# Optimization experiments

Measured on AMD Instinct MI355X. Metric: run time of the kernel, lower is better.

## Reference

```python
import jax, jax.numpy as jnp
import numpy as np

N = 50000   # nodes
E = 800000  # edges
IN = 128
H = 256
OUT = 10
G = 128     # graphs in batch


def _uniform(key, shape, fan_in):
    bound = 1.0 / np.sqrt(fan_in)
    return jax.random.uniform(key, shape, jnp.float32, -bound, bound)


def setup_inputs() -> dict:
    key = jax.random.key(0)
    ks = jax.random.split(key, 12)
    x = jax.random.normal(ks[0], (N, IN), jnp.float32)
    edge_index = jax.random.randint(ks[1], (2, E), 0, N, dtype=jnp.int64)
    edge_weight = jax.random.uniform(ks[2], (E,), jnp.float32)
    batch = jnp.sort(jax.random.randint(ks[3], (N,), 0, G, dtype=jnp.int64))
    # GCNConv weights (bias=False)
    W0 = _uniform(ks[4], (IN, H), IN)
    W1 = _uniform(ks[5], (H, H), H)
    W2 = _uniform(ks[6], (H, H), H)
    # MLP head: [H, H, OUT]
    Wm1 = _uniform(ks[7], (H, H), H)
    bm1 = _uniform(ks[8], (H,), H)
    Wm2 = _uniform(ks[9], (H, OUT), H)
    bm2 = _uniform(ks[10], (OUT,), H)
    return dict(x=x, edge_index=edge_index, edge_weight=edge_weight, batch=batch,
                W0=W0, W1=W1, W2=W2, Wm1=Wm1, bm1=bm1, Wm2=Wm2, bm2=bm2)


def _gcn_conv(h, W, row, col, dinv_sqrt):
    """GCNConv with self-loops and symmetric deg^-1/2 normalization, bias=False.
    Self-loop contribution handled analytically (norm = dinv_sqrt[i]^2)."""
    hw = h @ W                                        # [N, H]
    norm = dinv_sqrt[row] * dinv_sqrt[col]            # [E]
    msg = hw[row] * norm[:, None]                     # [E, H] gather-scale
    agg = jax.ops.segment_sum(msg, col, num_segments=N)  # scatter-add at targets
    return agg + (dinv_sqrt * dinv_sqrt)[:, None] * hw    # add self-loop term


def reference(x, edge_index, edge_weight, batch, W0, W1, W2, Wm1, bm1, Wm2, bm2):
    row, col = edge_index[0], edge_index[1]
    # degree including self-loop (edge_weight is ignored, as in the source)
    deg = jax.ops.segment_sum(jnp.ones((E,), x.dtype), col, num_segments=N) + 1.0
    dinv_sqrt = jax.lax.rsqrt(deg)
    h = x
    for W in (W0, W1, W2):
        h = jax.nn.relu(_gcn_conv(h, W, row, col, dinv_sqrt))
    # global mean pool over graphs
    counts = jax.ops.segment_sum(jnp.ones((N,), h.dtype), batch, num_segments=G)
    pooled = jax.ops.segment_sum(h, batch, num_segments=G) / jnp.maximum(counts, 1.0)[:, None]
    # MLP head (dropout inactive at inference)
    hmid = jax.nn.relu(pooled @ Wm1 + bm1)
    last = hmid @ Wm2 + bm2
    return jax.nn.log_softmax(last, axis=-1), jax.nn.sigmoid(last), last
```

## Files before the change

### kernel.cpp

```cpp
#include <hip/hip_runtime.h>
#include <math.h>

#define N_NODES 50000
#define N_PAD   50048
#define N_EDGES 800000
#define CSR_CAP 1200000
#define IN_F 128
#define H_F 256
#define OUT_F 10
#define N_G 128
#define NCHUNKS 196

#define HB 256
#define EPB (N_EDGES / HB)
#define HWORDS (N_NODES / 4)

typedef __attribute__((ext_vector_type(4))) float f32x4;
typedef __attribute__((ext_vector_type(2))) float f32x2;
typedef unsigned char u8;

__device__ inline f32x2 fp8x2_f32_lo(unsigned int v) {
    return __builtin_amdgcn_cvt_pk_f32_fp8(v, false);
}
__device__ inline f32x2 fp8x2_f32_hi(unsigned int v) {
    return __builtin_amdgcn_cvt_pk_f32_fp8(v, true);
}
__device__ inline unsigned int f32_fp8x2_lo(float a, float b, unsigned int old) {
    return __builtin_amdgcn_cvt_pk_fp8_f32(a, b, old, false);
}
__device__ inline unsigned int f32_fp8x2_hi(float a, float b, unsigned int old) {
    return __builtin_amdgcn_cvt_pk_fp8_f32(a, b, old, true);
}
__device__ inline u8 f32_fp8(float a) {
    return (u8)(f32_fp8x2_lo(a, a, 0u) & 0xff);
}
__device__ inline ushort f2bf(float x) {
    union { float f; unsigned int u; } v; v.f = x;
    unsigned int r = v.u + 0x7fff + ((v.u >> 16) & 1);
    return (ushort)(r >> 16);
}
__device__ inline float bf2f(ushort u) {
    union { unsigned int u; float f; } v; v.u = ((unsigned int)u) << 16; return v.f;
}

__device__ inline void gl2lds16(const void* g, void* l) {
    __builtin_amdgcn_global_load_lds(
        (const __attribute__((address_space(1))) unsigned int*)g,
        (__attribute__((address_space(3))) unsigned int*)l,
        16, 0, 0);
}

__global__ __launch_bounds__(256) void histo_kernel(const int* __restrict__ col,
                                                    u8* __restrict__ H) {
    extern __shared__ unsigned int hcnt[];
    int b = blockIdx.x;
    int tid = threadIdx.x;
    for (int j = tid; j < HWORDS; j += 256) hcnt[j] = 0u;
    __syncthreads();
    int e0 = b * EPB, e1 = e0 + EPB;
    for (int e = e0 + tid; e < e1; e += 512) {
        int c0 = col[e];
        int c1 = (e + 256 < e1) ? col[e + 256] : -1;
        atomicAdd(&hcnt[c0 >> 2], 1u << ((c0 & 3) << 3));
        if (c1 >= 0) atomicAdd(&hcnt[c1 >> 2], 1u << ((c1 & 3) << 3));
    }
    __syncthreads();
    unsigned int* Hrow = (unsigned int*)(H + (size_t)b * N_NODES);
    for (int j = tid; j < HWORDS; j += 256) Hrow[j] = hcnt[j];
}

#define CC_CHUNK 196
#define CC_X    (CC_CHUNK + 6250)
#define CC_T0   (CC_X + 128)
#define CC_T1   (CC_T0 + 256)
#define CC_T2   (CC_T1 + 256)
#define CC_GS   (CC_T2 + NCHUNKS)

__global__ __launch_bounds__(256) void convert_chunk_kernel(
    u8* __restrict__ H, int* __restrict__ counts, int* __restrict__ csum,
    const float* __restrict__ x, u8* __restrict__ xb,
    const float* __restrict__ W0, u8* __restrict__ W0t,
    const float* __restrict__ W1, u8* __restrict__ W1t,
    const float* __restrict__ W2, u8* __restrict__ W2t,
    const int* __restrict__ batch, int* __restrict__ gstart) {
    int b = blockIdx.x;
    int tid = threadIdx.x;
    if (b < CC_CHUNK) {
        int i = b * 256 + tid;
        int total = 0;
        if (i < N_NODES) {
            u8* ci = H + i;
            int s = 0;
            for (int b0 = 0; b0 < HB; b0 += 16) {
                int h[16];
                #pragma unroll
                for (int u = 0; u < 16; ++u)
                    h[u] = ci[(size_t)(b0 + u) * N_NODES];
                #pragma unroll
                for (int u = 0; u < 16; ++u) {
                    ci[(size_t)(b0 + u) * N_NODES] = (u8)s;
                    s += h[u];
                }
            }
            total = s;
            counts[i] = total;
        }
        int v = (i < N_NODES) ? ((total + 7) & ~7) : 0;
        #pragma unroll
        for (int off = 32; off; off >>= 1) v += __shfl_down(v, off);
        __shared__ int ws[4];
        if ((tid & 63) == 0) ws[tid >> 6] = v;
        __syncthreads();
        if (tid == 0) csum[b] = ws[0] + ws[1] + ws[2] + ws[3];
    } else if (b < CC_X) {
        int i = (b - CC_CHUNK) * 256 + tid;
        float4 v = *(const float4*)(x + (size_t)i * 4);
        unsigned int p = f32_fp8x2_lo(v.x, v.y, 0u);
        p = f32_fp8x2_hi(v.z, v.w, p);
        *(unsigned int*)(xb + (size_t)i * 4) = p;
    } else if (b < CC_T0) {
        int idx = (b - CC_X) * 256 + tid;
        int k = idx >> 8, nn = idx & 255;
        W0t[nn * IN_F + k] = f32_fp8(W0[idx]);
    } else if (b < CC_T1) {
        int idx = (b - CC_T0) * 256 + tid;
        int k = idx >> 8, nn = idx & 255;
        W1t[nn * H_F + k] = f32_fp8(W1[idx]);
    } else if (b < CC_T2) {
        int idx = (b - CC_T1) * 256 + tid;
        int k = idx >> 8, nn = idx & 255;
        W2t[nn * H_F + k] = f32_fp8(W2[idx]);
    } else {
        int i = (b - CC_T2) * 256 + tid;
        if (i >= N_NODES) return;
        int bb = batch[i];
        if (i == 0) {
            for (int g = 0; g <= bb; ++g) gstart[g] = 0;
        } else {
            int p = batch[i - 1];
            if (p != bb) { for (int g = p + 1; g <= bb; ++g) gstart[g] = i; }
        }
        if (i == N_NODES - 1) {
            for (int g = bb + 1; g <= N_G; ++g) gstart[g] = N_NODES;
        }
    }
}

__global__ __launch_bounds__(256) void scan_dinv_kernel(const int* __restrict__ counts,
                                                        const int* __restrict__ csum,
                                                        int* __restrict__ offsets,
                                                        float* __restrict__ dinv,
                                                        unsigned int* __restrict__ csr_ew,
                                                        int n) {
    int tid = threadIdx.x;
    int lane = tid & 63, wid = tid >> 6;
    int cv = (tid < NCHUNKS) ? csum[tid] : 0;
    int xc = cv;
    #pragma unroll
    for (int off = 1; off < 64; off <<= 1) {
        int t = __shfl_up(xc, off);
        if (lane >= off) xc += t;
    }
    __shared__ int cw[4], cpre[4];
    __shared__ int cexcl[257];
    if (lane == 63) cw[wid] = xc;
    __syncthreads();
    if (tid == 0) { int s = 0; for (int k = 0; k < 4; ++k) { cpre[k] = s; s += cw[k]; } }
    __syncthreads();
    cexcl[tid] = cpre[wid] + xc - cv;
    if (tid == 255) cexcl[256] = cpre[3] + cw[3];
    __syncthreads();
    int base = cexcl[blockIdx.x];
    int i = blockIdx.x * 256 + tid;
    int v = (i < n) ? counts[i] : 0;
    int pv = (v + 7) & ~7;
    int x = pv;
    #pragma unroll
    for (int off = 1; off < 64; off <<= 1) {
        int t = __shfl_up(x, off);
        if (lane >= off) x += t;
    }
    __shared__ int wsum[4], wpre[4];
    if (lane == 63) wsum[wid] = x;
    __syncthreads();
    if (tid == 0) { int s = 0; for (int k = 0; k < 4; ++k) { wpre[k] = s; s += wsum[k]; } }
    __syncthreads();
    if (i < n) {
        int o = base + wpre[wid] + x - pv;
        offsets[i] = o;
        dinv[i] = rsqrtf((float)(v + 1));
        for (int z = v; z < pv; ++z) csr_ew[o + z] = 0u;
    }
    if (blockIdx.x == 0 && tid == 0) offsets[n] = cexcl[NCHUNKS];
}

__global__ __launch_bounds__(256) void fill_csr_kernel(const int* __restrict__ row,
                                                       const int* __restrict__ col,
                                                       const int* __restrict__ offsets,
                                                       const u8* __restrict__ H,
                                                       const float* __restrict__ dinv,
                                                       unsigned int* __restrict__ csr_ew) {
    extern __shared__ unsigned int hl[];
    int b = blockIdx.x;
    int tid = threadIdx.x;
    const unsigned int* Hrow = (const unsigned int*)(H + (size_t)b * N_NODES);
    for (int j = tid; j < HWORDS; j += 256) hl[j] = Hrow[j];
    __syncthreads();
    int e0 = b * EPB, e1 = e0 + EPB;
    for (int e = e0 + tid; e < e1; e += 512) {
        int eb = e + 256;
        int c0 = col[e];
        int r0 = row[e];
        int c1 = -1, r1 = 0;
        if (eb < e1) { c1 = col[eb]; r1 = row[eb]; }
        float w0 = dinv[c0] * dinv[r0];
        float w1 = (c1 >= 0) ? dinv[c1] * dinv[r1] : 0.f;
        int sh0 = (c0 & 3) << 3;
        unsigned int old0 = atomicAdd(&hl[c0 >> 2], 1u << sh0);
        int k0 = (int)((old0 >> sh0) & 0xffu);
        csr_ew[offsets[c0] + k0] = (unsigned int)r0 | ((unsigned int)f2bf(w0) << 16);
        if (c1 >= 0) {
            int sh1 = (c1 & 3) << 3;
            unsigned int old1 = atomicAdd(&hl[c1 >> 2], 1u << sh1);
            int k1 = (int)((old1 >> sh1) & 0xffu);
            csr_ew[offsets[c1] + k1] = (unsigned int)r1 | ((unsigned int)f2bf(w1) << 16);
        }
    }
}

template <int K, bool RELU>
__global__ __launch_bounds__(256) void gemm_fp8(const u8* __restrict__ A,
                                                const u8* __restrict__ Bt,
                                                u8* __restrict__ C) {
    __shared__ u8 As[4 * 4096];
    __shared__ u8 Bs[4 * 4096];
    int tid = threadIdx.x;
    int lane = tid & 63;
    int w = tid >> 6;
    int wm = w & 1, wn = w >> 1;
    int l16 = lane & 15, quad = lane >> 4;
    int row0 = blockIdx.x * 128;
    int col0 = blockIdx.y * 128;
    f32x4 acc[4][4] = {};

    int sr = tid >> 1;
    int sh = (tid & 1) * 16;
    const u8* ga = A + (size_t)(row0 + sr) * K + sh;
    const u8* gb = Bt + (size_t)(col0 + sr) * K + sh;

    #pragma unroll
    for (int k0 = 0; k0 < K; k0 += 128) {
        if (k0) __syncthreads();
        #pragma unroll
        for (int q = 0; q < 4; ++q) {
            gl2lds16(ga + k0 + q * 32, As + q * 4096 + w * 1024);
            gl2lds16(gb + k0 + q * 32, Bs + q * 4096 + w * 1024);
        }
        __syncthreads();
        #pragma unroll
        for (int h = 0; h < 4; ++h) {
            long af[4], bfr[4];
            #pragma unroll
            for (int i = 0; i < 4; ++i)
                af[i] = *(const long*)&As[h * 4096 + (wm * 64 + i * 16 + l16) * 32 + quad * 8];
            #pragma unroll
            for (int j = 0; j < 4; ++j)
                bfr[j] = *(const long*)&Bs[h * 4096 + (wn * 64 + j * 16 + l16) * 32 + quad * 8];
            #pragma unroll
            for (int i = 0; i < 4; ++i)
                #pragma unroll
                for (int j = 0; j < 4; ++j)
                    acc[i][j] = __builtin_amdgcn_mfma_f32_16x16x32_fp8_fp8(af[i], bfr[j], acc[i][j], 0, 0, 0);
        }
    }
    #pragma unroll
    for (int i = 0; i < 4; ++i) {
        int rowb = row0 + wm * 64 + i * 16 + quad * 4;
        #pragma unroll
        for (int r = 0; r < 4; ++r) {
            int grow = rowb + r;
            #pragma unroll
            for (int j = 0; j < 4; ++j) {
                int gcol = col0 + wn * 64 + j * 16 + l16;
                float v = acc[i][j][r];
                if (RELU) v = fmaxf(v, 0.f);
                C[(size_t)grow * H_F + gcol] = f32_fp8(v);
            }
        }
    }
}

__global__ __launch_bounds__(256) void aggregate128(const u8* __restrict__ hw,
                                                    const float* __restrict__ dinv,
                                                    const int* __restrict__ offsets,
                                                    const unsigned int* __restrict__ csr_ew,
                                                    u8* __restrict__ hout) {
    int w = threadIdx.x >> 6;
    int lane = threadIdx.x & 63;
    int i = blockIdx.x * 4 + w;
    if (i >= N_NODES) return;
    float di = dinv[i];
    const u8* base = hw + (size_t)lane * 2;
    unsigned int su = *(const unsigned short*)(base + (size_t)i * IN_F);
    f32x2 sv = fp8x2_f32_lo(su);
    float s = di * di;
    float a0 = s * sv.x, a1 = s * sv.y;
    int t = __builtin_amdgcn_readfirstlane(offsets[i]);
    int end = __builtin_amdgcn_readfirstlane(offsets[i + 1]);
    if (t < end) {
        uint4 eA = *(const uint4*)(csr_ew + t);
        uint4 eB = *(const uint4*)(csr_ew + t + 4);
        for (; t < end; t += 8) {
            uint4 nA, nB;
            if (t + 8 < end) {
                nA = *(const uint4*)(csr_ew + t + 8);
                nB = *(const uint4*)(csr_ew + t + 12);
            }
            unsigned int e[8] = {eA.x, eA.y, eA.z, eA.w, eB.x, eB.y, eB.z, eB.w};
            unsigned int v[8];
            #pragma unroll
            for (int u = 0; u < 8; ++u)
                v[u] = *(const unsigned short*)(base + (size_t)(e[u] & 0xffff) * IN_F);
            #pragma unroll
            for (int u = 0; u < 8; ++u) {
                float wq = bf2f((ushort)(e[u] >> 16));
                f32x2 f = fp8x2_f32_lo(v[u]);
                a0 += wq * f.x; a1 += wq * f.y;
            }
            eA = nA; eB = nB;
        }
    }
    unsigned int o = f32_fp8x2_lo(a0, a1, 0u);
    *(unsigned short*)(hout + (size_t)i * IN_F + lane * 2) = (unsigned short)(o & 0xffff);
}

__global__ __launch_bounds__(256) void aggregate256(const u8* __restrict__ hw,
                                                    const float* __restrict__ dinv,
                                                    const int* __restrict__ offsets,
                                                    const unsigned int* __restrict__ csr_ew,
                                                    u8* __restrict__ hout) {
    int w = threadIdx.x >> 6;
    int lane = threadIdx.x & 63;
    int i = blockIdx.x * 4 + w;
    if (i >= N_NODES) return;
    float di = dinv[i];
    const u8* base = hw + (size_t)lane * 4;
    unsigned int su = *(const unsigned int*)(base + (size_t)i * H_F);
    f32x2 slo = fp8x2_f32_lo(su), shi = fp8x2_f32_hi(su);
    float s = di * di;
    float a0 = s * slo.x, a1 = s * slo.y, a2 = s * shi.x, a3 = s * shi.y;
    int t = __builtin_amdgcn_readfirstlane(offsets[i]);
    int end = __builtin_amdgcn_readfirstlane(offsets[i + 1]);
    if (t < end) {
        uint4 eA = *(const uint4*)(csr_ew + t);
        uint4 eB = *(const uint4*)(csr_ew + t + 4);
        for (; t < end; t += 8) {
            uint4 nA, nB;
            if (t + 8 < end) {
                nA = *(const uint4*)(csr_ew + t + 8);
                nB = *(const uint4*)(csr_ew + t + 12);
            }
            unsigned int e[8] = {eA.x, eA.y, eA.z, eA.w, eB.x, eB.y, eB.z, eB.w};
            unsigned int v[8];
            #pragma unroll
            for (int u = 0; u < 8; ++u)
                v[u] = *(const unsigned int*)(base + (size_t)(e[u] & 0xffff) * H_F);
            #pragma unroll
            for (int u = 0; u < 8; ++u) {
                float wq = bf2f((ushort)(e[u] >> 16));
                f32x2 lo = fp8x2_f32_lo(v[u]), hi = fp8x2_f32_hi(v[u]);
                a0 += wq * lo.x; a1 += wq * lo.y;
                a2 += wq * hi.x; a3 += wq * hi.y;
            }
            eA = nA; eB = nB;
        }
    }
    unsigned int o = f32_fp8x2_lo(fmaxf(a0, 0.f), fmaxf(a1, 0.f), 0u);
    o = f32_fp8x2_hi(fmaxf(a2, 0.f), fmaxf(a3, 0.f), o);
    *(unsigned int*)(hout + (size_t)i * H_F + lane * 4) = o;
}

__global__ __launch_bounds__(1024) void pool_mlp_kernel(const u8* __restrict__ h,
                                                        const int* __restrict__ gstart,
                                                        const float* __restrict__ Wm1,
                                                        const float* __restrict__ bm1,
                                                        const float* __restrict__ Wm2,
                                                        const float* __restrict__ bm2,
                                                        float* __restrict__ out) {
    __shared__ float sm[16][H_F];
    __shared__ float p[H_F];
    __shared__ float hmid[H_F];
    __shared__ float lastv[OUT_F];
    __shared__ float stats[2];
    int g = blockIdx.x;
    int s = gstart[g], e = gstart[g + 1];
    int w = threadIdx.x >> 6;
    int lane = threadIdx.x & 63;
    float a0 = 0.f, a1 = 0.f, a2 = 0.f, a3 = 0.f;
    for (int i = s + w; i < e; i += 16) {
        unsigned int v = *(const unsigned int*)(h + (size_t)i * H_F + lane * 4);
        f32x2 lo = fp8x2_f32_lo(v), hi = fp8x2_f32_hi(v);
        a0 += lo.x; a1 += lo.y; a2 += hi.x; a3 += hi.y;
    }
    *(f32x4*)&sm[w][lane * 4] = (f32x4){a0, a1, a2, a3};
    __syncthreads();
    int j = threadIdx.x;
    int cnt = e - s;
    if (j < H_F) {
        float t = 0.f;
        #pragma unroll
        for (int k = 0; k < 16; ++k) t += sm[k][j];
        p[j] = t / (float)max(cnt, 1);
    }
    __syncthreads();
    if (j < H_F) {
        float acc = bm1[j];
        for (int k = 0; k < H_F; ++k) acc += p[k] * Wm1[k * H_F + j];
        hmid[j] = fmaxf(acc, 0.f);
    }
    __syncthreads();
    if (j < OUT_F) {
        float a = bm2[j];
        for (int k = 0; k < H_F; ++k) a += hmid[k] * Wm2[k * OUT_F + j];
        lastv[j] = a;
    }
    __syncthreads();
    if (j == 0) {
        float m = -1e30f;
        for (int o = 0; o < OUT_F; ++o) m = fmaxf(m, lastv[o]);
        float sxp = 0.f;
        for (int o = 0; o < OUT_F; ++o) sxp += expf(lastv[o] - m);
        stats[0] = m; stats[1] = logf(sxp);
    }
    __syncthreads();
    if (j < OUT_F) {
        float v = lastv[j];
        out[g * OUT_F + j] = v - stats[0] - stats[1];
        out[(size_t)N_G * OUT_F + g * OUT_F + j] = 1.f / (1.f + expf(-v));
        out[(size_t)2 * N_G * OUT_F + g * OUT_F + j] = v;
    }
}

extern "C" void kernel_launch(void* const* d_in, const int* in_sizes, int n_in,
                              void* d_out, int out_size, void* d_ws, size_t ws_size,
                              hipStream_t stream) {
    const float* x   = (const float*)d_in[0];
    const int* edge_index = (const int*)d_in[1];
    const int* batch = (const int*)d_in[3];
    const float* W0  = (const float*)d_in[4];
    const float* W1  = (const float*)d_in[5];
    const float* W2  = (const float*)d_in[6];
    const float* Wm1 = (const float*)d_in[7];
    const float* bm1 = (const float*)d_in[8];
    const float* Wm2 = (const float*)d_in[9];
    const float* bm2 = (const float*)d_in[10];
    float* out = (float*)d_out;

    char* ws = (char*)d_ws;
    size_t off = 0;
    auto alloc = [&](size_t bytes) -> void* {
        void* p = ws + off; off += (bytes + 255) & ~(size_t)255; return p;
    };
    u8* xb       = (u8*)alloc((size_t)N_PAD * IN_F);
    u8* bufA     = (u8*)alloc((size_t)N_PAD * H_F);
    u8* bufB     = (u8*)alloc((size_t)N_PAD * H_F);
    u8* t0       = (u8*)alloc((size_t)N_PAD * IN_F);
    u8* W0t      = (u8*)alloc((size_t)H_F * IN_F);
    u8* W1t      = (u8*)alloc((size_t)H_F * H_F);
    u8* W2t      = (u8*)alloc((size_t)H_F * H_F);
    float* dinv    = (float*)alloc((size_t)N_NODES * 4);
    int*   counts  = (int*)alloc((size_t)N_NODES * 4);
    int*   offsets = (int*)alloc((size_t)(N_NODES + 1) * 4);
    u8*    H       = (u8*)alloc((size_t)HB * N_NODES);
    unsigned int* csr_ew = (unsigned int*)alloc((size_t)CSR_CAP * 4);
    int*   csum    = (int*)alloc((size_t)256 * 4);
    int*   gstart  = (int*)alloc((size_t)(N_G + 1) * 4);

    const int* row = edge_index;
    const int* col = edge_index + N_EDGES;

    histo_kernel<<<HB, 256, HWORDS * 4, stream>>>(col, H);
    convert_chunk_kernel<<<CC_GS, 256, 0, stream>>>(H, counts, csum, x, xb,
                                                    W0, W0t, W1, W1t, W2, W2t,
                                                    batch, gstart);
    scan_dinv_kernel<<<NCHUNKS, 256, 0, stream>>>(counts, csum, offsets, dinv,
                                                  csr_ew, N_NODES);
    fill_csr_kernel<<<HB, 256, HWORDS * 4, stream>>>(row, col, offsets, H,
                                                     dinv, csr_ew);

    dim3 gg(N_PAD / 128, H_F / 128);
    int agg_blocks = (N_NODES + 3) / 4;
    aggregate128<<<agg_blocks, 256, 0, stream>>>(xb, dinv, offsets, csr_ew, t0);
    gemm_fp8<IN_F, true><<<gg, 256, 0, stream>>>(t0, W0t, bufA);
    gemm_fp8<H_F, false><<<gg, 256, 0, stream>>>(bufA, W1t, bufB);
    aggregate256<<<agg_blocks, 256, 0, stream>>>(bufB, dinv, offsets, csr_ew, bufA);
    gemm_fp8<H_F, false><<<gg, 256, 0, stream>>>(bufA, W2t, bufB);
    aggregate256<<<agg_blocks, 256, 0, stream>>>(bufB, dinv, offsets, csr_ew, bufA);

    pool_mlp_kernel<<<N_G, 1024, 0, stream>>>(bufA, gstart, Wm1, bm1, Wm2, bm2, out);
}
```

Measured before the change: 267.6 us.

## Fuse CSR build kernels into one cooperative kernel with grid syncs

```diff
diff --git a/kernel.cpp b/kernel.cpp
--- a/kernel.cpp
+++ b/kernel.cpp
@@ -1,5 +1,8 @@
 #include <hip/hip_runtime.h>
+#include <hip/hip_cooperative_groups.h>
 #include <math.h>
+
+namespace cg = cooperative_groups;
 
 #define N_NODES 50000
 #define N_PAD   50048
@@ -14,6 +17,13 @@
 #define HB 256
 #define EPB (N_EDGES / HB)
 #define HWORDS (N_NODES / 4)
+#define COOP_GRID 512
+
+#define U_X   6250
+#define U_W0  (U_X + 128)
+#define U_W1  (U_W0 + 256)
+#define U_W2  (U_W1 + 256)
+#define U_GS  (U_W2 + NCHUNKS)
 
 typedef __attribute__((ext_vector_type(4))) float f32x4;
 typedef __attribute__((ext_vector_type(2))) float f32x2;
@@ -50,42 +60,75 @@
         16, 0, 0);
 }
 
-__global__ __launch_bounds__(256) void histo_kernel(const int* __restrict__ col,
-                                                    u8* __restrict__ H) {
-    extern __shared__ unsigned int hcnt[];
-    int b = blockIdx.x;
-    int tid = threadIdx.x;
-    for (int j = tid; j < HWORDS; j += 256) hcnt[j] = 0u;
-    __syncthreads();
-    int e0 = b * EPB, e1 = e0 + EPB;
-    for (int e = e0 + tid; e < e1; e += 512) {
-        int c0 = col[e];
-        int c1 = (e + 256 < e1) ? col[e + 256] : -1;
-        atomicAdd(&hcnt[c0 >> 2], 1u << ((c0 & 3) << 3));
-        if (c1 >= 0) atomicAdd(&hcnt[c1 >> 2], 1u << ((c1 & 3) << 3));
-    }
-    __syncthreads();
-    unsigned int* Hrow = (unsigned int*)(H + (size_t)b * N_NODES);
-    for (int j = tid; j < HWORDS; j += 256) Hrow[j] = hcnt[j];
-}
-
-#define CC_CHUNK 196
-#define CC_X    (CC_CHUNK + 6250)
-#define CC_T0   (CC_X + 128)
-#define CC_T1   (CC_T0 + 256)
-#define CC_T2   (CC_T1 + 256)
-#define CC_GS   (CC_T2 + NCHUNKS)
-
-__global__ __launch_bounds__(256) void convert_chunk_kernel(
+__global__ __launch_bounds__(256) void csr_build_kernel(
+    const int* __restrict__ col, const int* __restrict__ rowp,
     u8* __restrict__ H, int* __restrict__ counts, int* __restrict__ csum,
+    int* __restrict__ offsets, float* __restrict__ dinv,
+    unsigned int* __restrict__ csr_ew,
     const float* __restrict__ x, u8* __restrict__ xb,
     const float* __restrict__ W0, u8* __restrict__ W0t,
     const float* __restrict__ W1, u8* __restrict__ W1t,
     const float* __restrict__ W2, u8* __restrict__ W2t,
     const int* __restrict__ batch, int* __restrict__ gstart) {
+    extern __shared__ unsigned int lds[];
+    cg::grid_group grid = cg::this_grid();
     int b = blockIdx.x;
     int tid = threadIdx.x;
-    if (b < CC_CHUNK) {
+
+    if (b < HB) {
+        for (int j = tid; j < HWORDS; j += 256) lds[j] = 0u;
+        __syncthreads();
+        int e0 = b * EPB, e1 = e0 + EPB;
+        for (int e = e0 + tid; e < e1; e += 512) {
+            int c0 = col[e];
+            int c1 = (e + 256 < e1) ? col[e + 256] : -1;
+            atomicAdd(&lds[c0 >> 2], 1u << ((c0 & 3) << 3));
+            if (c1 >= 0) atomicAdd(&lds[c1 >> 2], 1u << ((c1 & 3) << 3));
+        }
+        __syncthreads();
+        unsigned int* Hrow = (unsigned int*)(H + (size_t)b * N_NODES);
+        for (int j = tid; j < HWORDS; j += 256) Hrow[j] = lds[j];
+    } else {
+        for (int unit = b - HB; unit < U_GS; unit += (COOP_GRID - HB)) {
+            if (unit < U_X) {
+                int i = unit * 256 + tid;
+                float4 v = *(const float4*)(x + (size_t)i * 4);
+                unsigned int p = f32_fp8x2_lo(v.x, v.y, 0u);
+                p = f32_fp8x2_hi(v.z, v.w, p);
+                *(unsigned int*)(xb + (size_t)i * 4) = p;
+            } else if (unit < U_W0) {
+                int idx = (unit - U_X) * 256 + tid;
+                int k = idx >> 8, nn = idx & 255;
+                W0t[nn * IN_F + k] = f32_fp8(W0[idx]);
+            } else if (unit < U_W1) {
+                int idx = (unit - U_W0) * 256 + tid;
+                int k = idx >> 8, nn = idx & 255;
+                W1t[nn * H_F + k] = f32_fp8(W1[idx]);
+            } else if (unit < U_W2) {
+                int idx = (unit - U_W1) * 256 + tid;
+                int k = idx >> 8, nn = idx & 255;
+                W2t[nn * H_F + k] = f32_fp8(W2[idx]);
+            } else {
+                int i = (unit - U_W2) * 256 + tid;
+                if (i < N_NODES) {
+                    int bb = batch[i];
+                    if (i == 0) {
+                        for (int g = 0; g <= bb; ++g) gstart[g] = 0;
+                    } else {
+                        int p = batch[i - 1];
+                        if (p != bb) { for (int g = p + 1; g <= bb; ++g) gstart[g] = i; }
+                    }
+                    if (i == N_NODES - 1) {
+                        for (int g = bb + 1; g <= N_G; ++g) gstart[g] = N_NODES;
+                    }
+                }
+            }
+        }
+    }
+    __threadfence();
+    grid.sync();
+
+    if (b < NCHUNKS) {
         int i = b * 256 + tid;
         int total = 0;
         if (i < N_NODES) {
@@ -112,118 +155,77 @@
         if ((tid & 63) == 0) ws[tid >> 6] = v;
         __syncthreads();
         if (tid == 0) csum[b] = ws[0] + ws[1] + ws[2] + ws[3];
-    } else if (b < CC_X) {
-        int i = (b - CC_CHUNK) * 256 + tid;
-        float4 v = *(const float4*)(x + (size_t)i * 4);
-        unsigned int p = f32_fp8x2_lo(v.x, v.y, 0u);
-        p = f32_fp8x2_hi(v.z, v.w, p);
-        *(unsigned int*)(xb + (size_t)i * 4) = p;
-    } else if (b < CC_T0) {
-        int idx = (b - CC_X) * 256 + tid;
-        int k = idx >> 8, nn = idx & 255;
-        W0t[nn * IN_F + k] = f32_fp8(W0[idx]);
-    } else if (b < CC_T1) {
-        int idx = (b - CC_T0) * 256 + tid;
-        int k = idx >> 8, nn = idx & 255;
-        W1t[nn * H_F + k] = f32_fp8(W1[idx]);
-    } else if (b < CC_T2) {
-        int idx = (b - CC_T1) * 256 + tid;
-        int k = idx >> 8, nn = idx & 255;
-        W2t[nn * H_F + k] = f32_fp8(W2[idx]);
-    } else {
-        int i = (b - CC_T2) * 256 + tid;
-        if (i >= N_NODES) return;
-        int bb = batch[i];
-        if (i == 0) {
-            for (int g = 0; g <= bb; ++g) gstart[g] = 0;
-        } else {
-            int p = batch[i - 1];
-            if (p != bb) { for (int g = p + 1; g <= bb; ++g) gstart[g] = i; }
-        }
-        if (i == N_NODES - 1) {
-            for (int g = bb + 1; g <= N_G; ++g) gstart[g] = N_NODES;
-        }
-    }
-}
-
-__global__ __launch_bounds__(256) void scan_dinv_kernel(const int* __restrict__ counts,
-                                                        const int* __restrict__ csum,
-                                                        int* __restrict__ offsets,
-                                                        float* __restrict__ dinv,
-                                                        unsigned int* __restrict__ csr_ew,
-                                                        int n) {
-    int tid = threadIdx.x;
-    int lane = tid & 63, wid = tid >> 6;
-    int cv = (tid < NCHUNKS) ? csum[tid] : 0;
-    int xc = cv;
-    #pragma unroll
-    for (int off = 1; off < 64; off <<= 1) {
-        int t = __shfl_up(xc, off);
-        if (lane >= off) xc += t;
-    }
-    __shared__ int cw[4], cpre[4];
-    __shared__ int cexcl[257];
-    if (lane == 63) cw[wid] = xc;
-    __syncthreads();
-    if (tid == 0) { int s = 0; for (int k = 0; k < 4; ++k) { cpre[k] = s; s += cw[k]; } }
-    __syncthreads();
-    cexcl[tid] = cpre[wid] + xc - cv;
-    if (tid == 255) cexcl[256] = cpre[3] + cw[3];
-    __syncthreads();
-    int base = cexcl[blockIdx.x];
-    int i = blockIdx.x * 256 + tid;
-    int v = (i < n) ? counts[i] : 0;
-    int pv = (v + 7) & ~7;
-    int x = pv;
-    #pragma unroll
-    for (int off = 1; off < 64; off <<= 1) {
-        int t = __shfl_up(x, off);
-        if (lane >= off) x += t;
-    }
-    __shared__ int wsum[4], wpre[4];
-    if (lane == 63) wsum[wid] = x;
-    __syncthreads();
-    if (tid == 0) { int s = 0; for (int k = 0; k < 4; ++k) { wpre[k] = s; s += wsum[k]; } }
-    __syncthreads();
-    if (i < n) {
-        int o = base + wpre[wid] + x - pv;
-        offsets[i] = o;
-        dinv[i] = rsqrtf((float)(v + 1));
-        for (int z = v; z < pv; ++z) csr_ew[o + z] = 0u;
-    }
-    if (blockIdx.x == 0 && tid == 0) offsets[n] = cexcl[NCHUNKS];
-}
-
-__global__ __launch_bounds__(256) void fill_csr_kernel(const int* __restrict__ row,
-                                                       const int* __restrict__ col,
-                                                       const int* __restrict__ offsets,
-                                                       const u8* __restrict__ H,
-                                                       const float* __restrict__ dinv,
-                                                       unsigned int* __restrict__ csr_ew) {
-    extern __shared__ unsigned int hl[];
-    int b = blockIdx.x;
-    int tid = threadIdx.x;
-    const unsigned int* Hrow = (const unsigned int*)(H + (size_t)b * N_NODES);
-    for (int j = tid; j < HWORDS; j += 256) hl[j] = Hrow[j];
-    __syncthreads();
-    int e0 = b * EPB, e1 = e0 + EPB;
-    for (int e = e0 + tid; e < e1; e += 512) {
-        int eb = e + 256;
-        int c0 = col[e];
-        int r0 = row[e];
-        int c1 = -1, r1 = 0;
-        if (eb < e1) { c1 = col[eb]; r1 = row[eb]; }
-        float w0 = dinv[c0] * dinv[r0];
-        float w1 = (c1 >= 0) ? dinv[c1] * dinv[r1] : 0.f;
-        int sh0 = (c0 & 3) << 3;
-        unsigned int old0 = atomicAdd(&hl[c0 >> 2], 1u << sh0);
-        int k0 = (int)((old0 >> sh0) & 0xffu);
-        csr_ew[offsets[c0] + k0] = (unsigned int)r0 | ((unsigned int)f2bf(w0) << 16);
-        if (c1 >= 0) {
-            int sh1 = (c1 & 3) << 3;
-            unsigned int old1 = atomicAdd(&hl[c1 >> 2], 1u << sh1);
-            int k1 = (int)((old1 >> sh1) & 0xffu);
-            csr_ew[offsets[c1] + k1] = (unsigned int)r1 | ((unsigned int)f2bf(w1) << 16);
+    }
+    __threadfence();
+    grid.sync();
+
+    if (b < NCHUNKS) {
+        int lane = tid & 63, wid = tid >> 6;
+        int cv = (tid < NCHUNKS) ? csum[tid] : 0;
+        int xc = cv;
+        #pragma unroll
+        for (int off = 1; off < 64; off <<= 1) {
+            int t = __shfl_up(xc, off);
+            if (lane >= off) xc += t;
+        }
+        __shared__ int cw[4], cpre[4];
+        __shared__ int cexcl[257];
+        if (lane == 63) cw[wid] = xc;
+        __syncthreads();
+        if (tid == 0) { int s = 0; for (int k = 0; k < 4; ++k) { cpre[k] = s; s += cw[k]; } }
+        __syncthreads();
+        cexcl[tid] = cpre[wid] + xc - cv;
+        if (tid == 255) cexcl[256] = cpre[3] + cw[3];
+        __syncthreads();
+        int base = cexcl[b];
+        int i = b * 256 + tid;
+        int v = (i < N_NODES) ? counts[i] : 0;
+        int pv = (v + 7) & ~7;
+        int xx = pv;
+        #pragma unroll
+        for (int off = 1; off < 64; off <<= 1) {
+            int t = __shfl_up(xx, off);
+            if (lane >= off) xx += t;
+        }
+        __shared__ int wsum[4], wpre[4];
+        if (lane == 63) wsum[wid] = xx;
+        __syncthreads();
+        if (tid == 0) { int s = 0; for (int k = 0; k < 4; ++k) { wpre[k] = s; s += wsum[k]; } }
+        __syncthreads();
+        if (i < N_NODES) {
+            int o = base + wpre[wid] + xx - pv;
+            offsets[i] = o;
+            dinv[i] = rsqrtf((float)(v + 1));
+            for (int z = v; z < pv; ++z) csr_ew[o + z] = 0u;
+        }
+        if (b == 0 && tid == 0) offsets[N_NODES] = cexcl[NCHUNKS];
+    }
+    __threadfence();
+    grid.sync();
+
+    if (b < HB) {
+        const unsigned int* Hrow = (const unsigned int*)(H + (size_t)b * N_NODES);
+        for (int j = tid; j < HWORDS; j += 256) lds[j] = Hrow[j];
+        __syncthreads();
+        int e0 = b * EPB, e1 = e0 + EPB;
+        for (int e = e0 + tid; e < e1; e += 512) {
+            int eb = e + 256;
+            int c0 = col[e];
+            int r0 = rowp[e];
+            int c1 = -1, r1 = 0;
+            if (eb < e1) { c1 = col[eb]; r1 = rowp[eb]; }
+            float w0 = dinv[c0] * dinv[r0];
+            float w1 = (c1 >= 0) ? dinv[c1] * dinv[r1] : 0.f;
+            int sh0 = (c0 & 3) << 3;
+            unsigned int old0 = atomicAdd(&lds[c0 >> 2], 1u << sh0);
+            int k0 = (int)((old0 >> sh0) & 0xffu);
+            csr_ew[offsets[c0] + k0] = (unsigned int)r0 | ((unsigned int)f2bf(w0) << 16);
+            if (c1 >= 0) {
+                int sh1 = (c1 & 3) << 3;
+                unsigned int old1 = atomicAdd(&lds[c1 >> 2], 1u << sh1);
+                int k1 = (int)((old1 >> sh1) & 0xffu);
+                csr_ew[offsets[c1] + k1] = (unsigned int)r1 | ((unsigned int)f2bf(w1) << 16);
+            }
         }
     }
 }
@@ -476,17 +478,19 @@
     int*   csum    = (int*)alloc((size_t)256 * 4);
     int*   gstart  = (int*)alloc((size_t)(N_G + 1) * 4);
 
-    const int* row = edge_index;
     const int* col = edge_index + N_EDGES;
-
-    histo_kernel<<<HB, 256, HWORDS * 4, stream>>>(col, H);
-    convert_chunk_kernel<<<CC_GS, 256, 0, stream>>>(H, counts, csum, x, xb,
-                                                    W0, W0t, W1, W1t, W2, W2t,
-                                                    batch, gstart);
-    scan_dinv_kernel<<<NCHUNKS, 256, 0, stream>>>(counts, csum, offsets, dinv,
-                                                  csr_ew, N_NODES);
-    fill_csr_kernel<<<HB, 256, HWORDS * 4, stream>>>(row, col, offsets, H,
-                                                     dinv, csr_ew);
+    const int* rowp = edge_index;
+
+    void* args[] = {
+        (void*)&col, (void*)&rowp, (void*)&H, (void*)&counts, (void*)&csum,
+        (void*)&offsets, (void*)&dinv, (void*)&csr_ew,
+        (void*)&x, (void*)&xb, (void*)&W0, (void*)&W0t,
+        (void*)&W1, (void*)&W1t, (void*)&W2, (void*)&W2t,
+        (void*)&batch, (void*)&gstart
+    };
+    hipLaunchCooperativeKernel((const void*)csr_build_kernel,
+                               dim3(COOP_GRID), dim3(256),
+                               args, HWORDS * 4, stream);
 
     dim3 gg(N_PAD / 128, H_F / 128);
     int agg_blocks = (N_NODES + 3) / 4;
```

Measured after the change: 631.1 us. +135.9%, slower.
